# Kernel tuning notes

Measured on AMD Instinct MI355X. Metric: run time of the kernel, lower is better.

The kernel has to match this reference:

```python
import jax, jax.numpy as jnp
import numpy as np

B, S, D_IN, UNITS = 8, 2048, 512, 512


def _glorot(key, fan_in, fan_out):
    limit = np.sqrt(6.0 / (fan_in + fan_out)).astype(np.float32)
    return jax.random.uniform(key, (fan_in, fan_out), jnp.float32, -limit, limit)


def setup_inputs() -> dict:
    key = jax.random.key(0)
    kq, kwq, kwv, kwk = jax.random.split(key, 4)
    return {
        "query": jax.random.normal(kq, (B, S, D_IN), jnp.float32),
        "Wq": _glorot(kwq, D_IN, UNITS),   # W_query conv1d k=1, no bias
        "Wv": _glorot(kwv, D_IN, UNITS),   # W_value conv1d k=1, no bias
        "Wk": _glorot(kwk, D_IN, UNITS),   # W_key   conv1d k=1, no bias
    }


def reference(query, Wq, Wv, Wk):
    # Pointwise causal Conv1D(kernel=1, no bias) with sigmoid activation == sigmoid(x @ W)
    q = jax.nn.sigmoid(jnp.einsum('bsd,du->bsu', query, Wq))   # W_query(query)
    k = jax.nn.sigmoid(jnp.einsum('bsd,du->bsu', query, Wv))   # W_value(key=query)
    v = jax.nn.sigmoid(jnp.einsum('bsd,du->bsu', query, Wk))   # W_key(value=query)

    d_in = query.shape[-1]  # scaling uses value's input feature dim, not units
    score = jnp.einsum('bqu,bku->bqk', q, k) / jnp.sqrt(jnp.float32(d_in))  # [B,S,S]

    # Mask: upper triangle INCLUDING diagonal is -inf (strictly-causal, no self)
    s = score.shape[1]
    masked = jnp.where(jnp.triu(jnp.ones((s, s), bool)), -jnp.inf, score)

    # Row 0 is fully masked -> replaced by zeros; rows 1: softmax over j < i
    rest = jax.nn.softmax(masked[:, 1:, :], axis=-1)
    attn = jnp.concatenate([jnp.zeros((score.shape[0], 1, s), score.dtype), rest], axis=1)

    return jnp.einsum('bqk,bku->bqu', attn, v)
```

## Files before the change

kernel.cpp:

```cpp
#include <hip/hip_runtime.h>
#include <stdint.h>


typedef __attribute__((ext_vector_type(4))) float f32x4;
typedef __attribute__((ext_vector_type(8))) short short8;
typedef __attribute__((ext_vector_type(4))) short short4b;

__device__ __forceinline__ short f2bf(float f) {
    union { float f; uint32_t u; } v; v.f = f;
    uint32_t r = (v.u + 0x7FFFu + ((v.u >> 16) & 1u)) >> 16;
    return (short)r;
}
__device__ __forceinline__ float bf2f(short s) {
    union { uint32_t u; float f; } v; v.u = ((uint32_t)(uint16_t)s) << 16; return v.f;
}
__device__ __forceinline__ float sigm(float x) { return 1.0f / (1.0f + __expf(-x)); }

__device__ __forceinline__ void gload_lds16(const void* g, void* l) {
    __builtin_amdgcn_global_load_lds(
        (const __attribute__((address_space(1))) void*)g,
        (__attribute__((address_space(3))) void*)l, 16, 0, 0);
}

#define VMBAR() asm volatile("s_waitcnt vmcnt(0)\n\ts_barrier" ::: "memory")

__global__ __launch_bounds__(256) void convert_x(
    const float* __restrict__ X, short* __restrict__ Xb)
{
    size_t i = (size_t)blockIdx.x * 256 + threadIdx.x;
    const float4* src = reinterpret_cast<const float4*>(X) + i * 2;
    float4 a = src[0], b = src[1];
    short8 o;
    o[0] = f2bf(a.x); o[1] = f2bf(a.y); o[2] = f2bf(a.z); o[3] = f2bf(a.w);
    o[4] = f2bf(b.x); o[5] = f2bf(b.y); o[6] = f2bf(b.z); o[7] = f2bf(b.w);
    *reinterpret_cast<short8*>(Xb + i * 8) = o;
}

__global__ __launch_bounds__(256) void prep_weights(
    const float* __restrict__ Wq, const float* __restrict__ Wv, const float* __restrict__ Wk,
    short* __restrict__ Wt)
{
    __shared__ float T[64 * 68];
    int bid = blockIdx.x;
    int w = bid >> 6;
    int tile = bid & 63;
    int n0 = (tile & 7) * 64;
    int k0 = (tile >> 3) * 64;
    const float* W = (w == 0) ? Wq : (w == 1) ? Wv : Wk;
    int t = threadIdx.x;
    int tr = t >> 4, tc = t & 15;
    for (int rr = 0; rr < 4; ++rr) {
        int row = rr * 16 + tr;
        float4 v = *reinterpret_cast<const float4*>(&W[(size_t)(k0 + row) * 512 + n0 + tc * 4]);
        T[row * 68 + tc * 4 + 0] = v.x;
        T[row * 68 + tc * 4 + 1] = v.y;
        T[row * 68 + tc * 4 + 2] = v.z;
        T[row * 68 + tc * 4 + 3] = v.w;
    }
    __syncthreads();
    for (int wr = 0; wr < 4; ++wr) {
        int nl = wr * 16 + tr;
        short4b o;
        for (int i = 0; i < 4; ++i) o[i] = f2bf(T[(tc * 4 + i) * 68 + nl]);
        *reinterpret_cast<short4b*>(&Wt[((size_t)(w * 512 + n0 + nl)) * 512 + k0 + tc * 4]) = o;
    }
}

__global__ __launch_bounds__(256, 2) void qkv_gemm(
    const short* __restrict__ Xb,
    const short* __restrict__ Wt,
    short* __restrict__ Qb, short* __restrict__ Kb, short* __restrict__ VtG)
{
    __shared__ short SMEM[2][16384];

    int bx = blockIdx.x;
    int mt = bx & 127;
    int y = bx >> 7;
    int w = y >> 2, nt = y & 3;
    int m0 = mt * 128, n0 = nt * 128;

    int tid = threadIdx.x;
    int wv = tid >> 6, lane = tid & 63;
    int wr = wv >> 1, wc = wv & 1;
    int ln = lane & 15, hi = lane >> 4;

    f32x4 acc[4][4];
#pragma unroll
    for (int i = 0; i < 4; ++i)
#pragma unroll
        for (int j = 0; j < 4; ++j) acc[i][j] = {0.f, 0.f, 0.f, 0.f};

    const short* Asrc = Xb + (size_t)m0 * 512;
    const short* Bsrc = Wt + (size_t)w * 512 * 512 + (size_t)n0 * 512;

    int srow = wv * 8 + (lane >> 3);
    int ssc0 = (lane & 7) * 8;

#define QSTAGE(ko, buf)                                                            \
    {                                                                              \
        int _k0 = (ko) * 64;                                                       \
        _Pragma("unroll")                                                          \
        for (int _j = 0; _j < 4; ++_j) {                                           \
            int _r = srow + _j * 32;                                               \
            int _sc = ssc0 ^ ((_r & 7) << 3);                                      \
            gload_lds16(Asrc + (size_t)_r * 512 + _k0 + _sc,                       \
                        &SMEM[buf][(wv * 8 + _j * 32) * 64]);                      \
        }                                                                          \
        _Pragma("unroll")                                                          \
        for (int _j = 0; _j < 4; ++_j) {                                           \
            int _r = srow + _j * 32;                                               \
            int _sc = ssc0 ^ ((_r & 7) << 3);                                      \
            gload_lds16(Bsrc + (size_t)_r * 512 + _k0 + _sc,                       \
                        &SMEM[buf][8192 + (wv * 8 + _j * 32) * 64]);               \
        }                                                                          \
    }

    QSTAGE(0, 0);
    for (int ko = 0; ko < 8; ++ko) {
        VMBAR();
        if (ko + 1 < 8) QSTAGE(ko + 1, (ko + 1) & 1);
        const short* As = SMEM[ko & 1];
        const short* Bs = SMEM[ko & 1] + 8192;
#pragma unroll
        for (int kk = 0; kk < 2; ++kk) {
            int kof = kk * 32 + hi * 8;
            int sw = (ln & 7) << 3;
            short8 af[4], bf[4];
#pragma unroll
            for (int mf = 0; mf < 4; ++mf)
                af[mf] = *reinterpret_cast<const short8*>(&As[(wr * 64 + mf * 16 + ln) * 64 + (kof ^ sw)]);
#pragma unroll
            for (int nf = 0; nf < 4; ++nf)
                bf[nf] = *reinterpret_cast<const short8*>(&Bs[(wc * 64 + nf * 16 + ln) * 64 + (kof ^ sw)]);
#pragma unroll
            for (int mf = 0; mf < 4; ++mf)
#pragma unroll
                for (int nf = 0; nf < 4; ++nf)
                    acc[mf][nf] = __builtin_amdgcn_mfma_f32_16x16x32_bf16(af[mf], bf[nf], acc[mf][nf], 0, 0, 0);
        }
    }
    __syncthreads();
#undef QSTAGE

    short* Ts = SMEM[0];
    if (w < 2) {
#pragma unroll
        for (int mf = 0; mf < 4; ++mf)
#pragma unroll
            for (int nf = 0; nf < 4; ++nf)
#pragma unroll
                for (int j = 0; j < 4; ++j) {
                    int rl = wr * 64 + mf * 16 + hi * 4 + j;
                    int cl = wc * 64 + nf * 16 + ln;
                    Ts[rl * 128 + (cl ^ ((rl & 7) << 3))] = f2bf(sigm(acc[mf][nf][j]));
                }
        __syncthreads();
        short* O = (w == 0) ? Qb : Kb;
        int r = tid >> 1, h = tid & 1;
#pragma unroll
        for (int i = 0; i < 8; ++i) {
            int c8 = h * 64 + i * 8;
            short8 v = *reinterpret_cast<const short8*>(&Ts[r * 128 + (c8 ^ ((r & 7) << 3))]);
            *reinterpret_cast<short8*>(&O[(size_t)(m0 + r) * 512 + n0 + c8]) = v;
        }
    } else {
#pragma unroll
        for (int mf = 0; mf < 4; ++mf)
#pragma unroll
            for (int nf = 0; nf < 4; ++nf)
#pragma unroll
                for (int j = 0; j < 4; ++j) {
                    int ml = wr * 64 + mf * 16 + hi * 4 + j;
                    int nl = wc * 64 + nf * 16 + ln;
                    Ts[nl * 128 + (ml ^ ((nl & 7) << 3))] = f2bf(sigm(acc[mf][nf][j]));
                }
        __syncthreads();
        int bb = m0 >> 11;
        int s0 = m0 & 2047;
        int d = tid >> 1, h = tid & 1;
#pragma unroll
        for (int i = 0; i < 8; ++i) {
            int s8 = h * 64 + i * 8;
            short8 v = *reinterpret_cast<const short8*>(&Ts[d * 128 + (s8 ^ ((d & 7) << 3))]);
            *reinterpret_cast<short8*>(&VtG[((size_t)(bb * 512 + n0 + d)) * 2048 + s0 + s8]) = v;
        }
    }
}

__global__ __launch_bounds__(256, 2) void score_pass(
    const short* __restrict__ Qb, const short* __restrict__ Kb,
    short* __restrict__ Pc, float* __restrict__ Dpart)
{
    __shared__ short SMEM[2][16384];
    __shared__ float psum[2][128];

    const float scale = 0.044194173824159216f;

    int bid = blockIdx.x;
    int b = bid & 7;
    int idx = bid >> 3;
    int ti = 0;
    while ((ti + 1) * (ti + 2) / 2 <= idx) ++ti;
    int tj = idx - ti * (ti + 1) / 2;
    int m0 = ti * 128, n0 = tj * 128;

    int tid = threadIdx.x;
    int w = tid >> 6, lane = tid & 63;
    int wr = w >> 1, wc = w & 1;
    int ln = lane & 15, hi = lane >> 4;

    const short* Qsrc = Qb + (size_t)b * 2048 * 512 + (size_t)m0 * 512;
    const short* Ksrc = Kb + (size_t)b * 2048 * 512 + (size_t)n0 * 512;

    f32x4 acc[4][4];
#pragma unroll
    for (int i = 0; i < 4; ++i)
#pragma unroll
        for (int j = 0; j < 4; ++j) acc[i][j] = {0.f, 0.f, 0.f, 0.f};

    int srow = w * 8 + (lane >> 3);
    int ssc0 = (lane & 7) * 8;

#define SSTAGE(ko, buf)                                                            \
    {                                                                              \
        int _k0 = (ko) * 64;                                                       \
        _Pragma("unroll")                                                          \
        for (int _j = 0; _j < 4; ++_j) {                                           \
            int _r = srow + _j * 32;                                               \
            int _sc = ssc0 ^ ((_r & 7) << 3);                                      \
            gload_lds16(Qsrc + (size_t)_r * 512 + _k0 + _sc,                       \
                        &SMEM[buf][(w * 8 + _j * 32) * 64]);                       \
        }                                                                          \
        _Pragma("unroll")                                                          \
        for (int _j = 0; _j < 4; ++_j) {                                           \
            int _r = srow + _j * 32;                                               \
            int _sc = ssc0 ^ ((_r & 7) << 3);                                      \
            gload_lds16(Ksrc + (size_t)_r * 512 + _k0 + _sc,                       \
                        &SMEM[buf][8192 + (w * 8 + _j * 32) * 64]);                \
        }                                                                          \
    }

    SSTAGE(0, 0);
    for (int ko = 0; ko < 8; ++ko) {
        VMBAR();
        if (ko + 1 < 8) SSTAGE(ko + 1, (ko + 1) & 1);
        const short* As = SMEM[ko & 1];
        const short* Bs = SMEM[ko & 1] + 8192;
#pragma unroll
        for (int kk = 0; kk < 2; ++kk) {
            int kof = kk * 32 + hi * 8;
            int sw = (ln & 7) << 3;
            short8 af[4], bf[4];
#pragma unroll
            for (int mf = 0; mf < 4; ++mf)
                af[mf] = *reinterpret_cast<const short8*>(&As[(wr * 64 + mf * 16 + ln) * 64 + (kof ^ sw)]);
#pragma unroll
            for (int nf = 0; nf < 4; ++nf)
                bf[nf] = *reinterpret_cast<const short8*>(&Bs[(wc * 64 + nf * 16 + ln) * 64 + (kof ^ sw)]);
#pragma unroll
            for (int mf = 0; mf < 4; ++mf)
#pragma unroll
                for (int nf = 0; nf < 4; ++nf)
                    acc[mf][nf] = __builtin_amdgcn_mfma_f32_16x16x32_bf16(af[mf], bf[nf], acc[mf][nf], 0, 0, 0);
        }
    }
    __syncthreads();
#undef SSTAGE

    short* Ts = SMEM[0];
#pragma unroll
    for (int mf = 0; mf < 4; ++mf) {
        float rs[4] = {0.f, 0.f, 0.f, 0.f};
#pragma unroll
        for (int nf = 0; nf < 4; ++nf)
#pragma unroll
            for (int j = 0; j < 4; ++j) {
                int rl = wr * 64 + mf * 16 + hi * 4 + j;
                int cl = wc * 64 + nf * 16 + ln;
                int irow = m0 + rl, jcol = n0 + cl;
                float p = (jcol < irow) ? __expf(acc[mf][nf][j] * scale) : 0.f;
                short hs = f2bf(p);
                Ts[rl * 128 + (cl ^ ((rl & 7) << 3))] = hs;
                rs[j] += bf2f(hs);
            }
#pragma unroll
        for (int j = 0; j < 4; ++j) {
            float s = rs[j];
            s += __shfl_xor(s, 1);
            s += __shfl_xor(s, 2);
            s += __shfl_xor(s, 4);
            s += __shfl_xor(s, 8);
            if (ln == 0) psum[wc][wr * 64 + mf * 16 + hi * 4 + j] = s;
        }
    }
    __syncthreads();
    short* Ptile = Pc + (size_t)(b * 136 + idx) * 128 * 128;
    {
        int r = tid >> 1, h = tid & 1;
#pragma unroll
        for (int i = 0; i < 8; ++i) {
            int c8 = h * 64 + i * 8;
            short8 v = *reinterpret_cast<const short8*>(&Ts[r * 128 + (c8 ^ ((r & 7) << 3))]);
            *reinterpret_cast<short8*>(&Ptile[(size_t)r * 128 + c8]) = v;
        }
    }
    if (tid < 128)
        Dpart[((size_t)b * 16 + tj) * 2048 + m0 + tid] = psum[0][tid] + psum[1][tid];
}

__global__ __launch_bounds__(256) void pv_pass(
    const short* __restrict__ Pc, const short* __restrict__ VtG,
    const float* __restrict__ Dpart, float* __restrict__ Out)
{
    __shared__ short SMEM[2][12288];
    __shared__ float dnm[128];

    int bid = blockIdx.x;
    int b = bid & 7;
    int rr = bid >> 3;
    int grp = rr >> 5, off = rr & 31;
    int ti = (grp & 1) ? (15 - (off >> 1)) : (off >> 1);
    int colhalf = 2 * grp + (off & 1);
    int m0 = ti * 128, n0 = colhalf * 64;

    int tid = threadIdx.x;
    int w = tid >> 6, lane = tid & 63;
    int wr = w >> 1, wc = w & 1;
    int ln = lane & 15, hi = lane >> 4;

    if (tid < 128) {
        float s = 0.f;
        for (int tj = 0; tj <= ti; ++tj)
            s += Dpart[((size_t)b * 16 + tj) * 2048 + m0 + tid];
        int gi = m0 + tid;
        dnm[tid] = (gi == 0) ? 0.f : 1.0f / s;
    }

    const short* Ptiles = Pc + (size_t)(b * 136 + ti * (ti + 1) / 2) * 128 * 128;
    const short* Vsrc = VtG + (size_t)b * 512 * 2048 + (size_t)n0 * 2048;

    f32x4 acc[4][2];
#pragma unroll
    for (int i = 0; i < 4; ++i)
#pragma unroll
        for (int j = 0; j < 2; ++j) acc[i][j] = {0.f, 0.f, 0.f, 0.f};

    int srow = w * 8 + (lane >> 3);
    int ssc0 = (lane & 7) * 8;
    int nks = 2 * (ti + 1);

#define PSTAGE(ks, buf)                                                            \
    {                                                                              \
        int _tj = (ks) >> 1;                                                       \
        int _j0 = ((ks) & 1) * 64;                                                 \
        const short* _Pt = Ptiles + (size_t)_tj * 128 * 128;                       \
        _Pragma("unroll")                                                          \
        for (int _j = 0; _j < 4; ++_j) {                                           \
            int _r = srow + _j * 32;                                               \
            int _sc = ssc0 ^ ((_r & 7) << 3);                                      \
            gload_lds16(_Pt + (size_t)_r * 128 + _j0 + _sc,                        \
                        &SMEM[buf][(w * 8 + _j * 32) * 64]);                       \
        }                                                                          \
        _Pragma("unroll")                                                          \
        for (int _j = 0; _j < 2; ++_j) {                                           \
            int _r = srow + _j * 32;                                               \
            int _sc = ssc0 ^ ((_r & 7) << 3);                                      \
            gload_lds16(Vsrc + (size_t)_r * 2048 + _tj * 128 + _j0 + _sc,          \
                        &SMEM[buf][8192 + (w * 8 + _j * 32) * 64]);                \
        }                                                                          \
    }

    PSTAGE(0, 0);
    for (int ks = 0; ks < nks; ++ks) {
        VMBAR();
        if (ks + 1 < nks) PSTAGE(ks + 1, (ks + 1) & 1);
        const short* As = SMEM[ks & 1];
        const short* Bs = SMEM[ks & 1] + 8192;
#pragma unroll
        for (int kk = 0; kk < 2; ++kk) {
            int kof = kk * 32 + hi * 8;
            int sw = (ln & 7) << 3;
            short8 af[4], bf[2];
#pragma unroll
            for (int mf = 0; mf < 4; ++mf)
                af[mf] = *reinterpret_cast<const short8*>(&As[(wr * 64 + mf * 16 + ln) * 64 + (kof ^ sw)]);
#pragma unroll
            for (int nf = 0; nf < 2; ++nf)
                bf[nf] = *reinterpret_cast<const short8*>(&Bs[(wc * 32 + nf * 16 + ln) * 64 + (kof ^ sw)]);
#pragma unroll
            for (int mf = 0; mf < 4; ++mf)
#pragma unroll
                for (int nf = 0; nf < 2; ++nf)
                    acc[mf][nf] = __builtin_amdgcn_mfma_f32_16x16x32_bf16(af[mf], bf[nf], acc[mf][nf], 0, 0, 0);
        }
    }
    __syncthreads();
#undef PSTAGE

    float* Tf = reinterpret_cast<float*>(SMEM);
#pragma unroll
    for (int mf = 0; mf < 4; ++mf)
#pragma unroll
        for (int nf = 0; nf < 2; ++nf)
#pragma unroll
            for (int j = 0; j < 4; ++j) {
                int rl = wr * 64 + mf * 16 + hi * 4 + j;
                int cl = wc * 32 + nf * 16 + ln;
                Tf[rl * 64 + (cl ^ ((rl & 7) << 2))] = acc[mf][nf][j] * dnm[rl];
            }
    __syncthreads();
    {
        int r = tid >> 1, h = tid & 1;
        float* orow = Out + ((size_t)b * 2048 + m0 + r) * 512 + n0;
#pragma unroll
        for (int i = 0; i < 8; ++i) {
            int c4 = (h * 8 + i) * 4;
            float4 v = *reinterpret_cast<const float4*>(&Tf[r * 64 + (c4 ^ ((r & 7) << 2))]);
            *reinterpret_cast<float4*>(&orow[c4]) = v;
        }
    }
}

extern "C" void kernel_launch(void* const* d_in, const int* in_sizes, int n_in,
                              void* d_out, int out_size, void* d_ws, size_t ws_size,
                              hipStream_t stream) {
    const float* X  = (const float*)d_in[0];
    const float* Wq = (const float*)d_in[1];
    const float* Wv = (const float*)d_in[2];
    const float* Wk = (const float*)d_in[3];
    float* Out = (float*)d_out;

    char* ws = (char*)d_ws;
    const size_t WT_BYTES  = (size_t)3 * 512 * 512 * 2;
    const size_t MAT_BYTES = (size_t)16384 * 512 * 2;
    const size_t PC_BYTES  = (size_t)8 * 136 * 128 * 128 * 2;
    short* Wt = (short*)ws;
    short* Qb = (short*)(ws + WT_BYTES);
    short* Kb = (short*)(ws + WT_BYTES + MAT_BYTES);
    short* Vt = (short*)(ws + WT_BYTES + 2 * MAT_BYTES);
    short* Pc = (short*)(ws + WT_BYTES + 3 * MAT_BYTES);
    short* Xb = Pc;
    float* Dp = (float*)(ws + WT_BYTES + 3 * MAT_BYTES + PC_BYTES);

    convert_x<<<4096, 256, 0, stream>>>(X, Xb);
    prep_weights<<<192, 256, 0, stream>>>(Wq, Wv, Wk, Wt);
    qkv_gemm<<<1536, 256, 0, stream>>>(Xb, Wt, Qb, Kb, Vt);
    score_pass<<<1088, 256, 0, stream>>>(Qb, Kb, Pc, Dp);
    pv_pass<<<1024, 256, 0, stream>>>(Pc, Vt, Dp, Out);
}
```

Measured before the change: 140.5 us.

## Keep X slab resident in LDS across all QKV tiles; fuse prep kernels

The QKV GEMM now launches one 512-thread block per 64-row slab of X. Each block loads the whole 64x512 bf16 slab into LDS once, then loops over all twelve 128-column weight tiles, double-buffering the weight slices and prefetching the next tile's first slice. This removes repeated X reloads and the 1536-block grid, but leaves each wave with a small 32x32 output tile and only one block per CU, so MFMA density and latency hiding may suffer. The X conversion and weight transpose kernels are also merged into a single launch to save one kernel dispatch.

```diff
diff --git a/kernel.cpp b/kernel.cpp
--- a/kernel.cpp
+++ b/kernel.cpp
@@ -24,24 +24,23 @@
 
 #define VMBAR() asm volatile("s_waitcnt vmcnt(0)\n\ts_barrier" ::: "memory")
 
-__global__ __launch_bounds__(256) void convert_x(
-    const float* __restrict__ X, short* __restrict__ Xb)
-{
-    size_t i = (size_t)blockIdx.x * 256 + threadIdx.x;
-    const float4* src = reinterpret_cast<const float4*>(X) + i * 2;
-    float4 a = src[0], b = src[1];
-    short8 o;
-    o[0] = f2bf(a.x); o[1] = f2bf(a.y); o[2] = f2bf(a.z); o[3] = f2bf(a.w);
-    o[4] = f2bf(b.x); o[5] = f2bf(b.y); o[6] = f2bf(b.z); o[7] = f2bf(b.w);
-    *reinterpret_cast<short8*>(Xb + i * 8) = o;
-}
-
-__global__ __launch_bounds__(256) void prep_weights(
-    const float* __restrict__ Wq, const float* __restrict__ Wv, const float* __restrict__ Wk,
-    short* __restrict__ Wt)
+__global__ __launch_bounds__(256) void fused_prep(
+    const float* __restrict__ X, const float* __restrict__ Wq,
+    const float* __restrict__ Wv, const float* __restrict__ Wk,
+    short* __restrict__ Xb, short* __restrict__ Wt)
 {
     __shared__ float T[64 * 68];
-    int bid = blockIdx.x;
+    if (blockIdx.x < 4096) {
+        size_t i = (size_t)blockIdx.x * 256 + threadIdx.x;
+        const float4* src = reinterpret_cast<const float4*>(X) + i * 2;
+        float4 a = src[0], b = src[1];
+        short8 o;
+        o[0] = f2bf(a.x); o[1] = f2bf(a.y); o[2] = f2bf(a.z); o[3] = f2bf(a.w);
+        o[4] = f2bf(b.x); o[5] = f2bf(b.y); o[6] = f2bf(b.z); o[7] = f2bf(b.w);
+        *reinterpret_cast<short8*>(Xb + i * 8) = o;
+        return;
+    }
+    int bid = blockIdx.x - 4096;
     int w = bid >> 6;
     int tile = bid & 63;
     int n0 = (tile & 7) * 64;
@@ -66,123 +65,131 @@
     }
 }
 
-__global__ __launch_bounds__(256, 2) void qkv_gemm(
+__global__ __launch_bounds__(512) void qkv_gemm(
     const short* __restrict__ Xb,
     const short* __restrict__ Wt,
     short* __restrict__ Qb, short* __restrict__ Kb, short* __restrict__ VtG)
 {
-    __shared__ short SMEM[2][16384];
-
-    int bx = blockIdx.x;
-    int mt = bx & 127;
-    int y = bx >> 7;
-    int w = y >> 2, nt = y & 3;
-    int m0 = mt * 128, n0 = nt * 128;
+    __shared__ short As[64 * 512];
+    __shared__ short Bs[2][128 * 64];
+    __shared__ short Ts[128 * 64];
+
+    int bid = blockIdx.x;
+    int m0 = bid * 64;
 
     int tid = threadIdx.x;
     int wv = tid >> 6, lane = tid & 63;
-    int wr = wv >> 1, wc = wv & 1;
+    int wm = wv >> 2, wn = wv & 3;
     int ln = lane & 15, hi = lane >> 4;
 
-    f32x4 acc[4][4];
-#pragma unroll
-    for (int i = 0; i < 4; ++i)
-#pragma unroll
-        for (int j = 0; j < 4; ++j) acc[i][j] = {0.f, 0.f, 0.f, 0.f};
-
-    const short* Asrc = Xb + (size_t)m0 * 512;
-    const short* Bsrc = Wt + (size_t)w * 512 * 512 + (size_t)n0 * 512;
-
-    int srow = wv * 8 + (lane >> 3);
-    int ssc0 = (lane & 7) * 8;
-
-#define QSTAGE(ko, buf)                                                            \
-    {                                                                              \
-        int _k0 = (ko) * 64;                                                       \
-        _Pragma("unroll")                                                          \
-        for (int _j = 0; _j < 4; ++_j) {                                           \
-            int _r = srow + _j * 32;                                               \
-            int _sc = ssc0 ^ ((_r & 7) << 3);                                      \
-            gload_lds16(Asrc + (size_t)_r * 512 + _k0 + _sc,                       \
-                        &SMEM[buf][(wv * 8 + _j * 32) * 64]);                      \
-        }                                                                          \
-        _Pragma("unroll")                                                          \
-        for (int _j = 0; _j < 4; ++_j) {                                           \
-            int _r = srow + _j * 32;                                               \
-            int _sc = ssc0 ^ ((_r & 7) << 3);                                      \
-            gload_lds16(Bsrc + (size_t)_r * 512 + _k0 + _sc,                       \
-                        &SMEM[buf][8192 + (wv * 8 + _j * 32) * 64]);               \
-        }                                                                          \
-    }
-
-    QSTAGE(0, 0);
-    for (int ko = 0; ko < 8; ++ko) {
-        VMBAR();
-        if (ko + 1 < 8) QSTAGE(ko + 1, (ko + 1) & 1);
-        const short* As = SMEM[ko & 1];
-        const short* Bs = SMEM[ko & 1] + 8192;
-#pragma unroll
-        for (int kk = 0; kk < 2; ++kk) {
-            int kof = kk * 32 + hi * 8;
-            int sw = (ln & 7) << 3;
-            short8 af[4], bf[4];
-#pragma unroll
-            for (int mf = 0; mf < 4; ++mf)
-                af[mf] = *reinterpret_cast<const short8*>(&As[(wr * 64 + mf * 16 + ln) * 64 + (kof ^ sw)]);
-#pragma unroll
-            for (int nf = 0; nf < 4; ++nf)
-                bf[nf] = *reinterpret_cast<const short8*>(&Bs[(wc * 64 + nf * 16 + ln) * 64 + (kof ^ sw)]);
-#pragma unroll
-            for (int mf = 0; mf < 4; ++mf)
-#pragma unroll
-                for (int nf = 0; nf < 4; ++nf)
-                    acc[mf][nf] = __builtin_amdgcn_mfma_f32_16x16x32_bf16(af[mf], bf[nf], acc[mf][nf], 0, 0, 0);
-        }
-    }
-    __syncthreads();
-#undef QSTAGE
-
-    short* Ts = SMEM[0];
-    if (w < 2) {
-#pragma unroll
-        for (int mf = 0; mf < 4; ++mf)
-#pragma unroll
-            for (int nf = 0; nf < 4; ++nf)
-#pragma unroll
-                for (int j = 0; j < 4; ++j) {
-                    int rl = wr * 64 + mf * 16 + hi * 4 + j;
-                    int cl = wc * 64 + nf * 16 + ln;
-                    Ts[rl * 128 + (cl ^ ((rl & 7) << 3))] = f2bf(sigm(acc[mf][nf][j]));
+    const short* Xsrc = Xb + (size_t)m0 * 512;
+
+#pragma unroll
+    for (int j = 0; j < 8; ++j) {
+        int r = wv * 8 + j;
+        const short* src = Xsrc + (size_t)r * 512 + ((lane * 8) ^ ((r & 7) << 3));
+        gload_lds16(src, &As[r * 512]);
+    }
+
+    auto stageB = [&](const short* Bsrc, int ko, int buf) {
+        int k0 = ko * 64;
+#pragma unroll
+        for (int j = 0; j < 2; ++j) {
+            int r0 = wv * 16 + j * 8;
+            int r = r0 + (lane >> 3);
+            const short* src = Bsrc + (size_t)r * 512 + k0 + (((lane & 7) * 8) ^ ((r & 7) << 3));
+            gload_lds16(src, &Bs[buf][r0 * 64]);
+        }
+    };
+
+    stageB(Wt, 0, 0);
+
+    for (int y = 0; y < 12; ++y) {
+        int w2 = y >> 2, nt = y & 3;
+        const short* Bsrc = Wt + (size_t)w2 * 512 * 512 + (size_t)(nt * 128) * 512;
+
+        f32x4 acc[2][2];
+#pragma unroll
+        for (int i = 0; i < 2; ++i)
+#pragma unroll
+            for (int j = 0; j < 2; ++j) acc[i][j] = {0.f, 0.f, 0.f, 0.f};
+
+        for (int ko = 0; ko < 8; ++ko) {
+            VMBAR();
+            if (ko + 1 < 8) {
+                stageB(Bsrc, ko + 1, (ko + 1) & 1);
+            } else if (y + 1 < 12) {
+                const short* Bn = Wt + (size_t)((y + 1) >> 2) * 512 * 512
+                                     + (size_t)(((y + 1) & 3) * 128) * 512;
+                stageB(Bn, 0, 0);
+            }
+            const short* Bc = Bs[ko & 1];
+            int kbase = ko * 64;
+#pragma unroll
+            for (int kk = 0; kk < 2; ++kk) {
+                int kof = kk * 32 + hi * 8;
+                short8 af[2], bf[2];
+#pragma unroll
+                for (int mf = 0; mf < 2; ++mf) {
+                    int r = wm * 32 + mf * 16 + ln;
+                    af[mf] = *reinterpret_cast<const short8*>(
+                        &As[r * 512 + ((kbase + kof) ^ ((r & 7) << 3))]);
                 }
-        __syncthreads();
-        short* O = (w == 0) ? Qb : Kb;
-        int r = tid >> 1, h = tid & 1;
-#pragma unroll
-        for (int i = 0; i < 8; ++i) {
-            int c8 = h * 64 + i * 8;
-            short8 v = *reinterpret_cast<const short8*>(&Ts[r * 128 + (c8 ^ ((r & 7) << 3))]);
-            *reinterpret_cast<short8*>(&O[(size_t)(m0 + r) * 512 + n0 + c8]) = v;
-        }
-    } else {
-#pragma unroll
-        for (int mf = 0; mf < 4; ++mf)
-#pragma unroll
-            for (int nf = 0; nf < 4; ++nf)
-#pragma unroll
-                for (int j = 0; j < 4; ++j) {
-                    int ml = wr * 64 + mf * 16 + hi * 4 + j;
-                    int nl = wc * 64 + nf * 16 + ln;
-                    Ts[nl * 128 + (ml ^ ((nl & 7) << 3))] = f2bf(sigm(acc[mf][nf][j]));
+#pragma unroll
+                for (int nf = 0; nf < 2; ++nf) {
+                    int r = wn * 32 + nf * 16 + ln;
+                    bf[nf] = *reinterpret_cast<const short8*>(
+                        &Bc[r * 64 + (kof ^ ((r & 7) << 3))]);
                 }
-        __syncthreads();
-        int bb = m0 >> 11;
-        int s0 = m0 & 2047;
-        int d = tid >> 1, h = tid & 1;
-#pragma unroll
-        for (int i = 0; i < 8; ++i) {
-            int s8 = h * 64 + i * 8;
-            short8 v = *reinterpret_cast<const short8*>(&Ts[d * 128 + (s8 ^ ((d & 7) << 3))]);
-            *reinterpret_cast<short8*>(&VtG[((size_t)(bb * 512 + n0 + d)) * 2048 + s0 + s8]) = v;
+#pragma unroll
+                for (int mf = 0; mf < 2; ++mf)
+#pragma unroll
+                    for (int nf = 0; nf < 2; ++nf)
+                        acc[mf][nf] = __builtin_amdgcn_mfma_f32_16x16x32_bf16(af[mf], bf[nf], acc[mf][nf], 0, 0, 0);
+            }
+        }
+
+        if (w2 < 2) {
+#pragma unroll
+            for (int mf = 0; mf < 2; ++mf)
+#pragma unroll
+                for (int nf = 0; nf < 2; ++nf)
+#pragma unroll
+                    for (int j = 0; j < 4; ++j) {
+                        int rl = wm * 32 + mf * 16 + hi * 4 + j;
+                        int cl = wn * 32 + nf * 16 + ln;
+                        Ts[rl * 128 + (cl ^ ((rl & 7) << 3))] = f2bf(sigm(acc[mf][nf][j]));
+                    }
+            __syncthreads();
+            short* O = (w2 == 0) ? Qb : Kb;
+            int r = tid >> 3, h = tid & 7;
+#pragma unroll
+            for (int i = 0; i < 2; ++i) {
+                int c8 = h * 16 + i * 8;
+                short8 v = *reinterpret_cast<const short8*>(&Ts[r * 128 + (c8 ^ ((r & 7) << 3))]);
+                *reinterpret_cast<short8*>(&O[(size_t)(m0 + r) * 512 + nt * 128 + c8]) = v;
+            }
+        } else {
+#pragma unroll
+            for (int mf = 0; mf < 2; ++mf)
+#pragma unroll
+                for (int nf = 0; nf < 2; ++nf)
+#pragma unroll
+                    for (int j = 0; j < 4; ++j) {
+                        int sl = wm * 32 + mf * 16 + hi * 4 + j;
+                        int dl = wn * 32 + nf * 16 + ln;
+                        Ts[dl * 64 + (sl ^ ((dl & 7) << 3))] = f2bf(sigm(acc[mf][nf][j]));
+                    }
+            __syncthreads();
+            int bb = m0 >> 11;
+            int s0 = m0 & 2047;
+            int d = tid >> 2, h = tid & 3;
+#pragma unroll
+            for (int i = 0; i < 2; ++i) {
+                int s8 = h * 16 + i * 8;
+                short8 v = *reinterpret_cast<const short8*>(&Ts[d * 64 + (s8 ^ ((d & 7) << 3))]);
+                *reinterpret_cast<short8*>(&VtG[((size_t)(bb * 512 + nt * 128 + d)) * 2048 + s0 + s8]) = v;
+            }
         }
     }
 }
@@ -442,9 +449,8 @@
     short* Xb = Pc;
     float* Dp = (float*)(ws + WT_BYTES + 3 * MAT_BYTES + PC_BYTES);
 
-    convert_x<<<4096, 256, 0, stream>>>(X, Xb);
-    prep_weights<<<192, 256, 0, stream>>>(Wq, Wv, Wk, Wt);
-    qkv_gemm<<<1536, 256, 0, stream>>>(Xb, Wt, Qb, Kb, Vt);
+    fused_prep<<<4288, 256, 0, stream>>>(X, Wq, Wv, Wk, Xb, Wt);
+    qkv_gemm<<<256, 512, 0, stream>>>(Xb, Wt, Qb, Kb, Vt);
     score_pass<<<1088, 256, 0, stream>>>(Qb, Kb, Pc, Dp);
     pv_pass<<<1024, 256, 0, stream>>>(Pc, Vt, Dp, Out);
 }
```

Result: slower. 174.2 us (+23.9%).

## Widen QKV GEMM tile to 128x256 with 512 threads and XCD-aware block mapping

Applied to the files above, without the earlier changes.

The fused QKV projection GEMM changes from 128x128 tiles with 4 waves to 128x256 tiles with 8 waves per block, so each loaded X tile is reused across twice as many output columns. The grid is halved. Block indices are also remapped so consecutive M tiles land on the same XCD, which should improve L2 reuse of X rows. The cost is a larger LDS footprint and one block per CU, which lowers occupancy and the ability to hide latency.

```diff
diff --git a/kernel.cpp b/kernel.cpp
--- a/kernel.cpp
+++ b/kernel.cpp
@@ -66,22 +66,24 @@
     }
 }
 
-__global__ __launch_bounds__(256, 2) void qkv_gemm(
+__global__ __launch_bounds__(512, 1) void qkv_gemm(
     const short* __restrict__ Xb,
     const short* __restrict__ Wt,
     short* __restrict__ Qb, short* __restrict__ Kb, short* __restrict__ VtG)
 {
-    __shared__ short SMEM[2][16384];
-
-    int bx = blockIdx.x;
-    int mt = bx & 127;
-    int y = bx >> 7;
-    int w = y >> 2, nt = y & 3;
-    int m0 = mt * 128, n0 = nt * 128;
+    __shared__ short SMEM[2][24576];
+
+    int bid = blockIdx.x;
+    int xcd = bid & 7;
+    int r5 = bid >> 3;
+    int mt = xcd * 16 + (r5 & 15);
+    int y2 = r5 >> 4;
+    int m0 = mt * 128;
+    int n2 = y2 * 256;
 
     int tid = threadIdx.x;
     int wv = tid >> 6, lane = tid & 63;
-    int wr = wv >> 1, wc = wv & 1;
+    int wm = wv >> 2, wn = wv & 3;
     int ln = lane & 15, hi = lane >> 4;
 
     f32x4 acc[4][4];
@@ -91,34 +93,33 @@
         for (int j = 0; j < 4; ++j) acc[i][j] = {0.f, 0.f, 0.f, 0.f};
 
     const short* Asrc = Xb + (size_t)m0 * 512;
-    const short* Bsrc = Wt + (size_t)w * 512 * 512 + (size_t)n0 * 512;
-
-    int srow = wv * 8 + (lane >> 3);
-    int ssc0 = (lane & 7) * 8;
-
-#define QSTAGE(ko, buf)                                                            \
+    const short* Bsrc = Wt + (size_t)n2 * 512;
+
+#define STAGE(ko, buf)                                                             \
     {                                                                              \
         int _k0 = (ko) * 64;                                                       \
         _Pragma("unroll")                                                          \
+        for (int _j = 0; _j < 2; ++_j) {                                           \
+            int _r0 = wv * 16 + _j * 8;                                            \
+            int _r = _r0 + (lane >> 3);                                            \
+            int _sc = ((lane & 7) * 8) ^ ((_r & 7) << 3);                          \
+            gload_lds16(Asrc + (size_t)_r * 512 + _k0 + _sc,                       \
+                        &SMEM[buf][_r0 * 64]);                                     \
+        }                                                                          \
+        _Pragma("unroll")                                                          \
         for (int _j = 0; _j < 4; ++_j) {                                           \
-            int _r = srow + _j * 32;                                               \
-            int _sc = ssc0 ^ ((_r & 7) << 3);                                      \
-            gload_lds16(Asrc + (size_t)_r * 512 + _k0 + _sc,                       \
-                        &SMEM[buf][(wv * 8 + _j * 32) * 64]);                      \
-        }                                                                          \
-        _Pragma("unroll")                                                          \
-        for (int _j = 0; _j < 4; ++_j) {                                           \
-            int _r = srow + _j * 32;                                               \
-            int _sc = ssc0 ^ ((_r & 7) << 3);                                      \
+            int _r0 = wv * 32 + _j * 8;                                            \
+            int _r = _r0 + (lane >> 3);                                            \
+            int _sc = ((lane & 7) * 8) ^ ((_r & 7) << 3);                          \
             gload_lds16(Bsrc + (size_t)_r * 512 + _k0 + _sc,                       \
-                        &SMEM[buf][8192 + (wv * 8 + _j * 32) * 64]);               \
-        }                                                                          \
-    }
-
-    QSTAGE(0, 0);
+                        &SMEM[buf][8192 + _r0 * 64]);                              \
+        }                                                                          \
+    }
+
+    STAGE(0, 0);
     for (int ko = 0; ko < 8; ++ko) {
         VMBAR();
-        if (ko + 1 < 8) QSTAGE(ko + 1, (ko + 1) & 1);
+        if (ko + 1 < 8) STAGE(ko + 1, (ko + 1) & 1);
         const short* As = SMEM[ko & 1];
         const short* Bs = SMEM[ko & 1] + 8192;
 #pragma unroll
@@ -127,11 +128,15 @@
             int sw = (ln & 7) << 3;
             short8 af[4], bf[4];
 #pragma unroll
-            for (int mf = 0; mf < 4; ++mf)
-                af[mf] = *reinterpret_cast<const short8*>(&As[(wr * 64 + mf * 16 + ln) * 64 + (kof ^ sw)]);
-#pragma unroll
-            for (int nf = 0; nf < 4; ++nf)
-                bf[nf] = *reinterpret_cast<const short8*>(&Bs[(wc * 64 + nf * 16 + ln) * 64 + (kof ^ sw)]);
+            for (int mf = 0; mf < 4; ++mf) {
+                int rr = wm * 64 + mf * 16 + ln;
+                af[mf] = *reinterpret_cast<const short8*>(&As[rr * 64 + (kof ^ sw)]);
+            }
+#pragma unroll
+            for (int nf = 0; nf < 4; ++nf) {
+                int rr = wn * 64 + nf * 16 + ln;
+                bf[nf] = *reinterpret_cast<const short8*>(&Bs[rr * 64 + (kof ^ sw)]);
+            }
 #pragma unroll
             for (int mf = 0; mf < 4; ++mf)
 #pragma unroll
@@ -140,28 +145,31 @@
         }
     }
     __syncthreads();
-#undef QSTAGE
-
+#undef STAGE
+
+    int w2 = n2 >> 9;
+    int nc = n2 & 511;
     short* Ts = SMEM[0];
-    if (w < 2) {
+
+    if (w2 < 2) {
 #pragma unroll
         for (int mf = 0; mf < 4; ++mf)
 #pragma unroll
             for (int nf = 0; nf < 4; ++nf)
 #pragma unroll
                 for (int j = 0; j < 4; ++j) {
-                    int rl = wr * 64 + mf * 16 + hi * 4 + j;
-                    int cl = wc * 64 + nf * 16 + ln;
-                    Ts[rl * 128 + (cl ^ ((rl & 7) << 3))] = f2bf(sigm(acc[mf][nf][j]));
+                    int rl = wm * 64 + mf * 16 + hi * 4 + j;
+                    int cl = wn * 64 + nf * 16 + ln;
+                    Ts[rl * 256 + (cl ^ ((rl & 7) << 3))] = f2bf(sigm(acc[mf][nf][j]));
                 }
         __syncthreads();
-        short* O = (w == 0) ? Qb : Kb;
-        int r = tid >> 1, h = tid & 1;
+        short* O = (w2 == 0) ? Qb : Kb;
+        int rr = tid >> 2, h = tid & 3;
 #pragma unroll
         for (int i = 0; i < 8; ++i) {
             int c8 = h * 64 + i * 8;
-            short8 v = *reinterpret_cast<const short8*>(&Ts[r * 128 + (c8 ^ ((r & 7) << 3))]);
-            *reinterpret_cast<short8*>(&O[(size_t)(m0 + r) * 512 + n0 + c8]) = v;
+            short8 v = *reinterpret_cast<const short8*>(&Ts[rr * 256 + (c8 ^ ((rr & 7) << 3))]);
+            *reinterpret_cast<short8*>(&O[(size_t)(m0 + rr) * 512 + nc + c8]) = v;
         }
     } else {
 #pragma unroll
@@ -170,9 +178,9 @@
             for (int nf = 0; nf < 4; ++nf)
 #pragma unroll
                 for (int j = 0; j < 4; ++j) {
-                    int ml = wr * 64 + mf * 16 + hi * 4 + j;
-                    int nl = wc * 64 + nf * 16 + ln;
-                    Ts[nl * 128 + (ml ^ ((nl & 7) << 3))] = f2bf(sigm(acc[mf][nf][j]));
+                    int sl = wm * 64 + mf * 16 + hi * 4 + j;
+                    int dl = wn * 64 + nf * 16 + ln;
+                    Ts[dl * 128 + (sl ^ ((dl & 7) << 3))] = f2bf(sigm(acc[mf][nf][j]));
                 }
         __syncthreads();
         int bb = m0 >> 11;
@@ -182,7 +190,7 @@
         for (int i = 0; i < 8; ++i) {
             int s8 = h * 64 + i * 8;
             short8 v = *reinterpret_cast<const short8*>(&Ts[d * 128 + (s8 ^ ((d & 7) << 3))]);
-            *reinterpret_cast<short8*>(&VtG[((size_t)(bb * 512 + n0 + d)) * 2048 + s0 + s8]) = v;
+            *reinterpret_cast<short8*>(&VtG[((size_t)(bb * 512 + nc + d)) * 2048 + s0 + s8]) = v;
         }
     }
 }
@@ -444,7 +452,7 @@
 
     convert_x<<<4096, 256, 0, stream>>>(X, Xb);
     prep_weights<<<192, 256, 0, stream>>>(Wq, Wv, Wk, Wt);
-    qkv_gemm<<<1536, 256, 0, stream>>>(Xb, Wt, Qb, Kb, Vt);
+    qkv_gemm<<<768, 512, 0, stream>>>(Xb, Wt, Qb, Kb, Vt);
     score_pass<<<1088, 256, 0, stream>>>(Qb, Kb, Pc, Dp);
     pv_pass<<<1024, 256, 0, stream>>>(Pc, Vt, Dp, Out);
 }
```

Result: slower. 153.2 us (+9.0%).
